# Kernel optimization log

Measured on AMD Instinct MI355X. Metric: run time of the kernel, lower is better.

The kernel has to match this reference:

```python
import jax, jax.numpy as jnp
import numpy as np

N, M, D = 16384, 4096, 128
NEG = -1e30  # masked-score fill


def setup_inputs() -> dict:
    key = jax.random.key(0)
    k1, k2, k3, k4 = jax.random.split(key, 4)
    self_feats = jax.random.normal(k1, (N, D), dtype=jnp.float32)
    features_neighs = jax.random.normal(k2, (M, D), dtype=jnp.float32)
    neigh_matrix = jax.random.randint(k3, (N, M), 0, 2, dtype=jnp.int32)
    # xavier_uniform for a: shape (2D, 1), gain=1 -> limit = sqrt(6/(2D+1))
    limit = float(np.sqrt(6.0 / (2 * D + 1)))
    a = jax.random.uniform(k4, (2 * D, 1), minval=-limit, maxval=limit, dtype=jnp.float32)
    return {"self_feats": self_feats, "features_neighs": features_neighs,
            "neigh_matrix": neigh_matrix, "a": a}


def reference(self_feats, features_neighs, neigh_matrix, a):
    # a = [a_self; a_neigh]; cat([self_i, neigh_j]) @ a = self_i@a_self + neigh_j@a_neigh
    d = self_feats.shape[1]
    s_self = self_feats @ a[:d, 0]        # [N]
    s_neigh = features_neighs @ a[d:, 0]  # [M]
    scores = jax.nn.leaky_relu(s_self[:, None] + s_neigh[None, :], 0.2)  # [N, M]
    mask = neigh_matrix.astype(bool)
    scores = jnp.where(mask, scores, NEG)
    attn = jax.nn.softmax(scores, axis=1)          # masked softmax per node
    attn = jnp.where(mask, attn, 0.0)              # nodes with no neighbors -> zeros
    return attn @ features_neighs                  # [N, D] weighted neighbor sum
```

## Files before the change

### kernel.cpp

```cpp
#include <hip/hip_runtime.h>
#include <hip/hip_bf16.h>

#define NROWS 16384
#define MCOLS 4096
#define DDIM  128
#define LOG2E 1.4426950408889634f

typedef __attribute__((ext_vector_type(8))) short short8;
typedef __attribute__((ext_vector_type(4))) float f32x4;

__device__ __forceinline__ float wave_reduce_add(float d) {
#pragma unroll
  for (int off = 32; off >= 1; off >>= 1) d += __shfl_xor(d, off, 64);
  return d;
}

__device__ __forceinline__ float pcalc(float t, int m) {
  float u = fmaxf(t, 0.2f * t);
  float e = exp2f(u);
  return m != 0 ? e : 0.f;
}

__device__ __forceinline__ unsigned short f2bf(float f) {
  unsigned u = __builtin_bit_cast(unsigned, f);
  return (unsigned short)((u + 0x7fffu + ((u >> 16) & 1u)) >> 16);
}

__device__ __forceinline__ unsigned pack_bf2(float lo, float hi) {
  return (unsigned)f2bf(lo) | ((unsigned)f2bf(hi) << 16);
}

__global__ __launch_bounds__(256) void aggr_prep(
    const float* __restrict__ V, const float* __restrict__ a,
    float* __restrict__ sneigh, short* __restrict__ packedV) {
  const int t = threadIdx.x, lane = t & 63, w = t >> 6;
  const int blk = blockIdx.x;

  float a0 = a[DDIM + 2 * lane] * LOG2E;
  float a1 = a[DDIM + 2 * lane + 1] * LOG2E;
#pragma unroll
  for (int i = 0; i < 4; ++i) {
    int j = blk * 16 + w * 4 + i;
    float2 v = *(const float2*)(V + (long)j * DDIM + 2 * lane);
    float d = wave_reduce_add(v.x * a0 + v.y * a1);
    if (lane == 0) sneigh[j] = d;
  }

  const int tg = blk * 256 + t;
  const int l = tg & 63;
  const int chunkid = tg >> 6;
  const int c = chunkid & 15, kt = chunkid >> 4;
  const int ks2 = c >> 3, cf = c & 7;
  const int col = cf * 16 + (l & 15);
  const long krow = (long)kt * 64 + ks2 * 32 + (l >> 4) * 8;
  short8 o;
#pragma unroll
  for (int b = 0; b < 8; ++b) {
    float f = V[(krow + b) * DDIM + col];
    o[b] = (short)f2bf(f);
  }
  *(short8*)(packedV + (long)tg * 8) = o;
}

__global__ __launch_bounds__(512, 2) void aggr_main(
    const float* __restrict__ self_feats, const int* __restrict__ nm,
    const float* __restrict__ a, const float* __restrict__ sneigh,
    const short* __restrict__ packedV, float* __restrict__ out) {
  __shared__ float s_sn[MCOLS];
  __shared__ float s_ss[64];
  __shared__ __align__(16) short Bst[2][2][8192];
  __shared__ float comb[4][16][132];
  __shared__ float den_x[64];
  __shared__ float den_f[64];

  const int t = threadIdx.x, lane = t & 63, w = t >> 6;
  const int rw = w & 3, ks = w >> 2;
  const int blk = blockIdx.x;
  const int rowblk = blk * 64;
  const int arow = lane & 15, kg = lane >> 4;

  {
    float a0 = a[2 * lane] * LOG2E, a1 = a[2 * lane + 1] * LOG2E;
#pragma unroll
    for (int i = 0; i < 8; ++i) {
      int r = w * 8 + i;
      float2 v = *(const float2*)(self_feats + (long)(rowblk + r) * DDIM + 2 * lane);
      float d = wave_reduce_add(v.x * a0 + v.y * a1);
      if (lane == 0) s_ss[r] = d;
    }
  }
  {
    const float4* src = (const float4*)sneigh;
    float4* dst = (float4*)s_sn;
    dst[t] = src[t];
    dst[t + 512] = src[t + 512];
  }

  auto STAGE = [&](int buf, int it2) {
    int ktn = it2 * 2 + ks;
#pragma unroll
    for (int j = 0; j < 4; ++j) {
      int c = (w & 3) * 4 + j;
      const short* g = packedV + ((long)(ktn * 16 + c) * 64 + lane) * 8;
      __builtin_amdgcn_global_load_lds(
          (const __attribute__((address_space(1))) void*)g,
          (__attribute__((address_space(3))) void*)(&Bst[buf][ks][c * 512]),
          16, 0, 0);
    }
  };

  const int* mbase = nm + (long)(rowblk + rw * 16 + arow) * MCOLS + kg * 8;

  int4 mc[4], mn[4] = {};
  STAGE(0, 0);
  {
    const int kt0 = ks;
#pragma unroll
    for (int ks2 = 0; ks2 < 2; ++ks2)
#pragma unroll
      for (int q = 0; q < 2; ++q)
        mc[ks2 * 2 + q] = *(const int4*)(mbase + kt0 * 64 + ks2 * 32 + q * 4);
  }
  __syncthreads();

  const float si = s_ss[rw * 16 + arow];

  f32x4 acc[8];
#pragma unroll
  for (int i = 0; i < 8; ++i) acc[i] = (f32x4){0.f, 0.f, 0.f, 0.f};
  float den = 0.f;

  for (int it = 0; it < 32; ++it) {
    const int kt = it * 2 + ks;
    const int buf = it & 1;
    if (it < 31) {
      STAGE(buf ^ 1, it + 1);
      const int ktn = (it + 1) * 2 + ks;
#pragma unroll
      for (int ks2 = 0; ks2 < 2; ++ks2)
#pragma unroll
        for (int q = 0; q < 2; ++q)
          mn[ks2 * 2 + q] = *(const int4*)(mbase + ktn * 64 + ks2 * 32 + q * 4);
    }

    short8 afr[2];
#pragma unroll
    for (int ks2 = 0; ks2 < 2; ++ks2) {
      const float* sj = &s_sn[kt * 64 + ks2 * 32 + kg * 8];
      float4 s0 = *(const float4*)sj;
      float4 s1 = *(const float4*)(sj + 4);
      int4 m0 = mc[ks2 * 2], m1 = mc[ks2 * 2 + 1];
      float p0 = pcalc(si + s0.x, m0.x);
      float p1 = pcalc(si + s0.y, m0.y);
      float p2 = pcalc(si + s0.z, m0.z);
      float p3 = pcalc(si + s0.w, m0.w);
      float p4 = pcalc(si + s1.x, m1.x);
      float p5 = pcalc(si + s1.y, m1.y);
      float p6 = pcalc(si + s1.z, m1.z);
      float p7 = pcalc(si + s1.w, m1.w);
      den += ((p0 + p1) + (p2 + p3)) + ((p4 + p5) + (p6 + p7));
      int4 ai;
      ai.x = (int)pack_bf2(p0, p1);
      ai.y = (int)pack_bf2(p2, p3);
      ai.z = (int)pack_bf2(p4, p5);
      ai.w = (int)pack_bf2(p6, p7);
      afr[ks2] = __builtin_bit_cast(short8, ai);
    }

    const short8* Bks = (const short8*)&Bst[buf][ks][0];
#pragma unroll
    for (int cf = 0; cf < 8; ++cf) {
      acc[cf] = __builtin_amdgcn_mfma_f32_16x16x32_bf16(afr[0], Bks[cf * 64 + lane], acc[cf], 0, 0, 0);
      acc[cf] = __builtin_amdgcn_mfma_f32_16x16x32_bf16(afr[1], Bks[(8 + cf) * 64 + lane], acc[cf], 0, 0, 0);
    }

    __syncthreads();
    if (it < 31) { mc[0] = mn[0]; mc[1] = mn[1]; mc[2] = mn[2]; mc[3] = mn[3]; }
  }

  den += __shfl_xor(den, 16, 64);
  den += __shfl_xor(den, 32, 64);

  if (ks == 1) {
#pragma unroll
    for (int cf = 0; cf < 8; ++cf)
#pragma unroll
      for (int r = 0; r < 4; ++r)
        comb[rw][kg * 4 + r][cf * 16 + arow] = acc[cf][r];
    if (lane < 16) den_x[rw * 16 + lane] = den;
  }
  __syncthreads();
  if (ks == 0) {
    float dtot = den + den_x[rw * 16 + arow];
    if (lane < 16) den_f[rw * 16 + lane] = dtot;
  }
  __syncthreads();
  if (ks == 0) {
    float rcp[4];
#pragma unroll
    for (int r = 0; r < 4; ++r) {
      float dv = den_f[rw * 16 + kg * 4 + r];
      rcp[r] = dv > 0.f ? 1.0f / dv : 0.f;
    }
#pragma unroll
    for (int cf = 0; cf < 8; ++cf)
#pragma unroll
      for (int r = 0; r < 4; ++r) {
        float v = (acc[cf][r] + comb[rw][kg * 4 + r][cf * 16 + arow]) * rcp[r];
        out[(long)(rowblk + rw * 16 + kg * 4 + r) * DDIM + cf * 16 + arow] = v;
      }
  }
}

extern "C" void kernel_launch(void* const* d_in, const int* in_sizes, int n_in,
                              void* d_out, int out_size, void* d_ws, size_t ws_size,
                              hipStream_t stream) {
  const float* self_feats = (const float*)d_in[0];
  const float* V = (const float*)d_in[1];
  const int* nm = (const int*)d_in[2];
  const float* a = (const float*)d_in[3];
  float* out = (float*)d_out;

  float* sneigh = (float*)d_ws;
  short* packedV = (short*)((char*)d_ws + 16384);

  aggr_prep<<<256, 256, 0, stream>>>(V, a, sneigh, packedV);
  aggr_main<<<256, 512, 0, stream>>>(self_feats, nm, a, sneigh, packedV, out);
}
```

Measured before the change: 402.6 us.

## Pre-pack int32 neighbor mask into a bitmask before the main aggregation kernel

Adds a separate streaming kernel that turns the 256 MB int32 adjacency matrix into a 1-bit-per-entry bitmask (8 MB) in workspace. The main attention kernel then reads one 64-bit word per iteration instead of four int4 loads, and extracts per-column bits with shifts. This takes the large mask stream out of the compute and MFMA pipeline, where it competed with staging and latency hiding, and cuts register pressure from the prefetched mask. The cost is an extra kernel launch and a round trip for the 8 MB bitmask, while the full mask read still happens in the pack kernel.

```diff
diff --git a/kernel.cpp b/kernel.cpp
--- a/kernel.cpp
+++ b/kernel.cpp
@@ -8,6 +8,7 @@
 
 typedef __attribute__((ext_vector_type(8))) short short8;
 typedef __attribute__((ext_vector_type(4))) float f32x4;
+typedef unsigned long long u64;
 
 __device__ __forceinline__ float wave_reduce_add(float d) {
 #pragma unroll
@@ -28,6 +29,26 @@
 
 __device__ __forceinline__ unsigned pack_bf2(float lo, float hi) {
   return (unsigned)f2bf(lo) | ((unsigned)f2bf(hi) << 16);
+}
+
+__global__ __launch_bounds__(256) void aggr_pack(
+    const int4* __restrict__ nm4, u64* __restrict__ bm64) {
+  __shared__ unsigned char sB[2048];
+  const int t = threadIdx.x;
+  const long blk = blockIdx.x;
+#pragma unroll
+  for (int j = 0; j < 8; ++j) {
+    int4 a = nm4[blk * 4096 + j * 512 + t * 2];
+    int4 b = nm4[blk * 4096 + j * 512 + t * 2 + 1];
+    unsigned byte =
+        (a.x != 0 ? 1u : 0u) | (a.y != 0 ? 2u : 0u) | (a.z != 0 ? 4u : 0u) |
+        (a.w != 0 ? 8u : 0u) | (b.x != 0 ? 16u : 0u) | (b.y != 0 ? 32u : 0u) |
+        (b.z != 0 ? 64u : 0u) | (b.w != 0 ? 128u : 0u);
+    sB[j * 256 + t] = (unsigned char)byte;
+  }
+  __syncthreads();
+  u64 w = *(const u64*)&sB[t * 8];
+  bm64[blk * 256 + t] = w;
 }
 
 __global__ __launch_bounds__(256) void aggr_prep(
@@ -63,7 +84,7 @@
 }
 
 __global__ __launch_bounds__(512, 2) void aggr_main(
-    const float* __restrict__ self_feats, const int* __restrict__ nm,
+    const float* __restrict__ self_feats, const unsigned char* __restrict__ bm,
     const float* __restrict__ a, const float* __restrict__ sneigh,
     const short* __restrict__ packedV, float* __restrict__ out) {
   __shared__ float s_sn[MCOLS];
@@ -109,18 +130,11 @@
     }
   };
 
-  const int* mbase = nm + (long)(rowblk + rw * 16 + arow) * MCOLS + kg * 8;
-
-  int4 mc[4], mn[4] = {};
+  const unsigned char* bmrow = bm + (long)(rowblk + rw * 16 + arow) * 512;
+
+  u64 mu_c, mu_n = 0;
   STAGE(0, 0);
-  {
-    const int kt0 = ks;
-#pragma unroll
-    for (int ks2 = 0; ks2 < 2; ++ks2)
-#pragma unroll
-      for (int q = 0; q < 2; ++q)
-        mc[ks2 * 2 + q] = *(const int4*)(mbase + kt0 * 64 + ks2 * 32 + q * 4);
-  }
+  mu_c = *(const u64*)(bmrow + ks * 8);
   __syncthreads();
 
   const float si = s_ss[rw * 16 + arow];
@@ -135,12 +149,7 @@
     const int buf = it & 1;
     if (it < 31) {
       STAGE(buf ^ 1, it + 1);
-      const int ktn = (it + 1) * 2 + ks;
-#pragma unroll
-      for (int ks2 = 0; ks2 < 2; ++ks2)
-#pragma unroll
-        for (int q = 0; q < 2; ++q)
-          mn[ks2 * 2 + q] = *(const int4*)(mbase + ktn * 64 + ks2 * 32 + q * 4);
+      mu_n = *(const u64*)(bmrow + ((it + 1) * 2 + ks) * 8);
     }
 
     short8 afr[2];
@@ -149,15 +158,15 @@
       const float* sj = &s_sn[kt * 64 + ks2 * 32 + kg * 8];
       float4 s0 = *(const float4*)sj;
       float4 s1 = *(const float4*)(sj + 4);
-      int4 m0 = mc[ks2 * 2], m1 = mc[ks2 * 2 + 1];
-      float p0 = pcalc(si + s0.x, m0.x);
-      float p1 = pcalc(si + s0.y, m0.y);
-      float p2 = pcalc(si + s0.z, m0.z);
-      float p3 = pcalc(si + s0.w, m0.w);
-      float p4 = pcalc(si + s1.x, m1.x);
-      float p5 = pcalc(si + s1.y, m1.y);
-      float p6 = pcalc(si + s1.z, m1.z);
-      float p7 = pcalc(si + s1.w, m1.w);
+      unsigned mb = (unsigned)(mu_c >> (ks2 * 32 + kg * 8)) & 0xffu;
+      float p0 = pcalc(si + s0.x, (int)(mb & 1u));
+      float p1 = pcalc(si + s0.y, (int)(mb & 2u));
+      float p2 = pcalc(si + s0.z, (int)(mb & 4u));
+      float p3 = pcalc(si + s0.w, (int)(mb & 8u));
+      float p4 = pcalc(si + s1.x, (int)(mb & 16u));
+      float p5 = pcalc(si + s1.y, (int)(mb & 32u));
+      float p6 = pcalc(si + s1.z, (int)(mb & 64u));
+      float p7 = pcalc(si + s1.w, (int)(mb & 128u));
       den += ((p0 + p1) + (p2 + p3)) + ((p4 + p5) + (p6 + p7));
       int4 ai;
       ai.x = (int)pack_bf2(p0, p1);
@@ -175,7 +184,7 @@
     }
 
     __syncthreads();
-    if (it < 31) { mc[0] = mn[0]; mc[1] = mn[1]; mc[2] = mn[2]; mc[3] = mn[3]; }
+    mu_c = mu_n;
   }
 
   den += __shfl_xor(den, 16, 64);
@@ -222,8 +231,11 @@
   float* out = (float*)d_out;
 
   float* sneigh = (float*)d_ws;
-  short* packedV = (short*)((char*)d_ws + 16384);
-
+  short* packedV = (short*)((char*)d_ws + (1 << 14));
+  u64* bm64 = (u64*)((char*)d_ws + (1 << 21));
+
+  aggr_pack<<<4096, 256, 0, stream>>>((const int4*)nm, bm64);
   aggr_prep<<<256, 256, 0, stream>>>(V, a, sneigh, packedV);
-  aggr_main<<<256, 512, 0, stream>>>(self_feats, nm, a, sneigh, packedV, out);
-}
+  aggr_main<<<256, 512, 0, stream>>>(self_feats, (const unsigned char*)bm64,
+                                     a, sneigh, packedV, out);
+}
```

Result: slower. 421.7 us (+4.7%).
